# Kernel optimization log

Hardware: AMD Instinct MI355X
Metric: run time of the kernel (lower is better)

Reference implementation:

```python
import jax, jax.numpy as jnp
import numpy as np

B, N, D = 16, 32768, 256
E, H, K, T = 512, 8, 512, 16  # text_embed_dim, nhead, top_k, num_defect_tokens
LN_EPS = 1e-5


def setup_inputs() -> dict:
    key = jax.random.key(0)
    ks = jax.random.split(key, 8)
    sc = 0.02
    return {
        "per_point_features": jax.random.normal(ks[0], (B, N, D), jnp.float32),
        "outlier_scores": jax.random.normal(ks[1], (B, N, 1), jnp.float32),
        "proj_w": jax.random.normal(ks[2], (E, D), jnp.float32) * sc,
        "proj_b": jnp.zeros((E,), jnp.float32),
        "in_proj_w": jax.random.normal(ks[3], (3 * E, E), jnp.float32) * sc,
        "in_proj_b": jnp.zeros((3 * E,), jnp.float32),
        "out_proj_w": jax.random.normal(ks[4], (E, E), jnp.float32) * sc,
        "out_proj_b": jnp.zeros((E,), jnp.float32),
        "ln_g": jnp.ones((E,), jnp.float32),
        "ln_b": jnp.zeros((E,), jnp.float32),
        "ffn_w": jax.random.normal(ks[5], (E, E), jnp.float32) * sc,
        "ffn_b": jnp.zeros((E,), jnp.float32),
    }


def _layernorm(x, g, b):
    mu = jnp.mean(x, axis=-1, keepdims=True)
    var = jnp.mean(jnp.square(x - mu), axis=-1, keepdims=True)
    return (x - mu) * jax.lax.rsqrt(var + LN_EPS) * g + b


def reference(per_point_features, outlier_scores, proj_w, proj_b,
              in_proj_w, in_proj_b, out_proj_w, out_proj_b,
              ln_g, ln_b, ffn_w, ffn_b):
    # top-k select + gather
    scores = outlier_scores[..., 0]                       # [B, N]
    _, idx = jax.lax.top_k(scores, K)                     # [B, K]
    feats = jnp.take_along_axis(per_point_features, idx[:, :, None], axis=1)  # [B, K, D]
    # linear projection to text embed dim
    x = feats @ proj_w.T + proj_b                         # [B, K, E]
    # multi-head self-attention (torch nn.MultiheadAttention semantics)
    qkv = x @ in_proj_w.T + in_proj_b                     # [B, K, 3E]
    q, k, v = jnp.split(qkv, 3, axis=-1)
    dh = E // H
    q = q.reshape(B, K, H, dh)
    k = k.reshape(B, K, H, dh)
    v = v.reshape(B, K, H, dh)
    logits = jnp.einsum("bqhd,bkhd->bhqk", q, k) / np.sqrt(dh).astype(np.float32)
    attn = jax.nn.softmax(logits, axis=-1)
    o = jnp.einsum("bhqk,bkhd->bqhd", attn, v).reshape(B, K, E)
    o = o @ out_proj_w.T + out_proj_b
    # residual + layernorm
    y = _layernorm(x + o, ln_g, ln_b)
    # FFN (linear + exact GELU) with residual
    y = y + jax.nn.gelu(y @ ffn_w.T + ffn_b, approximate=False)
    return y[:, :T, :]                                    # [B, T, E]
```

## Files before the change

kernel.cpp:

```cpp
#include <hip/hip_runtime.h>
#include <hip/hip_bf16.h>
#include <math.h>

#define PB 16
#define PN 32768
#define PD 256
#define PE 512
#define PH 8
#define PK 512
#define PT 16
#define DH 64

typedef __attribute__((ext_vector_type(8))) short bf16x8;
typedef __attribute__((ext_vector_type(4))) float f32x4;

__device__ __forceinline__ unsigned short f2bf(float f) {
    __hip_bfloat16 h = __float2bfloat16(f);
    return *(unsigned short*)&h;
}
__device__ __forceinline__ float b2f(unsigned short u) {
    return __uint_as_float(((unsigned int)u) << 16);
}

__global__ __launch_bounds__(512) void topk_kernel(const float* __restrict__ scores,
                                                   int* __restrict__ sorted_idx) {
    const int b = blockIdx.x;
    const int tid = threadIdx.x;
    const int NT = 512;
    const float* s = scores + (size_t)b * PN;

    __shared__ unsigned int hist[256];
    __shared__ unsigned int sh_prefix;
    __shared__ int sh_remaining;
    __shared__ unsigned int sh_cnt_gt, sh_cnt_eq;
    __shared__ unsigned long long comp[PK];
    __shared__ unsigned int eq_idx[PK];

    unsigned int prefix = 0;
    int remaining = PK;
    for (int shift = 24; shift >= 0; shift -= 8) {
        for (int i = tid; i < 256; i += NT) hist[i] = 0;
        __syncthreads();
        for (int i = tid * 4; i < PN; i += NT * 4) {
            float4 f = *(const float4*)(s + i);
            const float* fp = (const float*)&f;
#pragma unroll
            for (int j = 0; j < 4; ++j) {
                unsigned int u = __float_as_uint(fp[j]);
                u = (u & 0x80000000u) ? ~u : (u | 0x80000000u);
                bool ok = (shift == 24) || ((u >> (shift + 8)) == prefix);
                if (ok) atomicAdd(&hist[(u >> shift) & 0xFFu], 1u);
            }
        }
        __syncthreads();
        if (tid == 0) {
            int cum = 0;
            int d = 255;
            for (; d >= 0; --d) {
                cum += (int)hist[d];
                if (cum >= remaining) break;
            }
            sh_remaining = remaining - (cum - (int)hist[d]);
            sh_prefix = (prefix << 8) | (unsigned)d;
        }
        __syncthreads();
        prefix = sh_prefix;
        remaining = sh_remaining;
        __syncthreads();
    }
    const unsigned int TKEY = prefix;

    if (tid == 0) { sh_cnt_gt = 0; sh_cnt_eq = 0; }
    __syncthreads();
    for (int i = tid * 4; i < PN; i += NT * 4) {
        float4 f = *(const float4*)(s + i);
        const float* fp = (const float*)&f;
#pragma unroll
        for (int j = 0; j < 4; ++j) {
            unsigned int u = __float_as_uint(fp[j]);
            u = (u & 0x80000000u) ? ~u : (u | 0x80000000u);
            if (u > TKEY) {
                unsigned p = atomicAdd(&sh_cnt_gt, 1u);
                comp[p] = ((unsigned long long)u << 32) | (unsigned int)(~(unsigned)(i + j));
            } else if (u == TKEY) {
                unsigned p = atomicAdd(&sh_cnt_eq, 1u);
                if (p < PK) eq_idx[p] = (unsigned)(i + j);
            }
        }
    }
    __syncthreads();
    const int cnt_gt = (int)sh_cnt_gt;
    const int need_eq = PK - cnt_gt;
    const int ec = (int)sh_cnt_eq < PK ? (int)sh_cnt_eq : PK;
    if (tid == 0) {
        for (int j = 0; j < need_eq; ++j) {
            unsigned mv = 0xFFFFFFFFu; int mb = 0;
            for (int i2 = 0; i2 < ec; ++i2)
                if (eq_idx[i2] < mv) { mv = eq_idx[i2]; mb = i2; }
            comp[cnt_gt + j] = ((unsigned long long)TKEY << 32) | (unsigned int)(~mv);
            eq_idx[mb] = 0xFFFFFFFFu;
        }
    }
    __syncthreads();

    for (unsigned ksz = 2; ksz <= PK; ksz <<= 1) {
        for (unsigned j = ksz >> 1; j > 0; j >>= 1) {
            unsigned i = (unsigned)tid;
            unsigned ixj = i ^ j;
            if (ixj > i && i < PK) {
                unsigned long long a = comp[i], c = comp[ixj];
                bool sw = ((i & ksz) == 0) ? (a < c) : (a > c);
                if (sw) { comp[i] = c; comp[ixj] = a; }
            }
            __syncthreads();
        }
    }
    if (tid < PK)
        sorted_idx[b * PK + tid] = (int)(~(unsigned int)(comp[tid] & 0xFFFFFFFFull));
}

__global__ __launch_bounds__(256) void gather_cast_kernel(const float* __restrict__ feats,
                                                          const int* __restrict__ sidx,
                                                          __hip_bfloat16* __restrict__ Ag) {
    const int row = blockIdx.x * 4 + (threadIdx.x >> 6);
    const int lane = threadIdx.x & 63;
    const int b = row >> 9;
    const int src = sidx[row];
    float4 f = *(const float4*)(feats + ((size_t)b * PN + (size_t)src) * PD + lane * 4);
    ushort4 u;
    u.x = f2bf(f.x); u.y = f2bf(f.y); u.z = f2bf(f.z); u.w = f2bf(f.w);
    *(ushort4*)((unsigned short*)Ag + (size_t)row * PD + lane * 4) = u;
}

__global__ __launch_bounds__(256) void cast_weights_kernel(
    const float* __restrict__ proj_w, const float* __restrict__ kv_w,
    __hip_bfloat16* __restrict__ Wp16, __hip_bfloat16* __restrict__ Wkv16) {
    const int n1 = PE * PD / 4;
    const int n2 = 2 * PE * PE / 4;
    int i = blockIdx.x * 256 + threadIdx.x;
    const float4* src;
    unsigned short* dst;
    int off;
    if (i < n1) { src = (const float4*)proj_w; dst = (unsigned short*)Wp16; off = i; }
    else if (i < n1 + n2) { src = (const float4*)kv_w; dst = (unsigned short*)Wkv16; off = i - n1; }
    else return;
    float4 f = src[off];
    ushort4 u;
    u.x = f2bf(f.x); u.y = f2bf(f.y); u.z = f2bf(f.z); u.w = f2bf(f.w);
    *(ushort4*)(dst + (size_t)off * 4) = u;
}

__global__ __launch_bounds__(256) void gemm_bt_bf16_kernel(
    const short* __restrict__ A, const short* __restrict__ Bm,
    const float* __restrict__ bias,
    __hip_bfloat16* __restrict__ C16, float* __restrict__ Xq,
    int M, int N, int Kd) {
    const int tid = threadIdx.x;
    const int wave = tid >> 6;
    const int lane = tid & 63;
    const int m0 = blockIdx.x * 128 + (wave >> 1) * 64;
    const int n0 = blockIdx.y * 128 + (wave & 1) * 64;
    const int mrow = lane & 15;
    const int quad = lane >> 4;

    f32x4 acc[4][4] = {};
    for (int k0 = 0; k0 < Kd; k0 += 32) {
        const int kk = k0 + quad * 8;
        bf16x8 a[4], bf[4];
#pragma unroll
        for (int i = 0; i < 4; ++i)
            a[i] = *(const bf16x8*)(A + (size_t)(m0 + i * 16 + mrow) * Kd + kk);
#pragma unroll
        for (int i = 0; i < 4; ++i)
            bf[i] = *(const bf16x8*)(Bm + (size_t)(n0 + i * 16 + mrow) * Kd + kk);
#pragma unroll
        for (int i = 0; i < 4; ++i)
#pragma unroll
            for (int j = 0; j < 4; ++j)
                acc[i][j] = __builtin_amdgcn_mfma_f32_16x16x32_bf16(a[i], bf[j], acc[i][j], 0, 0, 0);
    }
#pragma unroll
    for (int i = 0; i < 4; ++i)
#pragma unroll
        for (int j = 0; j < 4; ++j)
#pragma unroll
            for (int r = 0; r < 4; ++r) {
                int row = m0 + i * 16 + quad * 4 + r;
                int col = n0 + j * 16 + mrow;
                float v = acc[i][j][r] + bias[col];
                if (C16) {
                    __hip_bfloat16 hv = __float2bfloat16(v);
                    ((__hip_bfloat16*)C16)[(size_t)row * N + col] = hv;
                }
                if (Xq) {
                    int t = row & (PK - 1);
                    if (t < PT)
                        Xq[((size_t)(row >> 9) * PT + t) * N + col] = v;
                }
            }
}

__global__ __launch_bounds__(256) void sgemm_bt_kernel(
    const float* __restrict__ A, const float* __restrict__ Bm,
    const float* __restrict__ bias, const float* __restrict__ resid,
    float* __restrict__ C, int M, int N, int Kd) {
    __shared__ float As[32][33];
    __shared__ float Bs[32][33];
    const int tid = threadIdx.x;
    const int m0 = blockIdx.x * 32, n0 = blockIdx.y * 32;
    const int tx = tid & 15, ty = tid >> 4;
    float acc00 = 0, acc01 = 0, acc10 = 0, acc11 = 0;
    for (int k0 = 0; k0 < Kd; k0 += 32) {
        for (int e = tid; e < 1024; e += 256) {
            int r = e >> 5, c = e & 31;
            As[r][c] = A[(size_t)(m0 + r) * Kd + k0 + c];
            Bs[r][c] = Bm[(size_t)(n0 + r) * Kd + k0 + c];
        }
        __syncthreads();
#pragma unroll
        for (int kk = 0; kk < 32; ++kk) {
            float a0 = As[ty * 2][kk], a1 = As[ty * 2 + 1][kk];
            float b0 = Bs[tx * 2][kk], b1 = Bs[tx * 2 + 1][kk];
            acc00 += a0 * b0; acc01 += a0 * b1;
            acc10 += a1 * b0; acc11 += a1 * b1;
        }
        __syncthreads();
    }
    float bc0 = bias[n0 + tx * 2], bc1 = bias[n0 + tx * 2 + 1];
    float v00 = acc00 + bc0, v01 = acc01 + bc1, v10 = acc10 + bc0, v11 = acc11 + bc1;
    size_t i00 = (size_t)(m0 + ty * 2) * N + n0 + tx * 2;
    size_t i10 = (size_t)(m0 + ty * 2 + 1) * N + n0 + tx * 2;
    if (resid) {
        v00 = resid[i00]     + 0.5f * v00 * (1.0f + erff(v00 * 0.7071067811865475f));
        v01 = resid[i00 + 1] + 0.5f * v01 * (1.0f + erff(v01 * 0.7071067811865475f));
        v10 = resid[i10]     + 0.5f * v10 * (1.0f + erff(v10 * 0.7071067811865475f));
        v11 = resid[i10 + 1] + 0.5f * v11 * (1.0f + erff(v11 * 0.7071067811865475f));
    }
    C[i00] = v00; C[i00 + 1] = v01;
    C[i10] = v10; C[i10 + 1] = v11;
}

__global__ __launch_bounds__(256) void attn_kernel(
    const float* __restrict__ qb, const __hip_bfloat16* __restrict__ kv,
    float* __restrict__ ob) {
    const int bh = blockIdx.x;
    const int b = bh >> 3, h = bh & 7;
    const int tid = threadIdx.x;
    __shared__ float qs[PT][DH + 4];
    __shared__ float ls[PT][PK + 1];

    {
        int i4 = tid * 4;
        int t = i4 >> 6, d = i4 & 63;
        float4 f = *(const float4*)(qb + (size_t)(b * PT + t) * PE + h * DH + d);
        qs[t][d] = f.x; qs[t][d + 1] = f.y; qs[t][d + 2] = f.z; qs[t][d + 3] = f.w;
    }
    __syncthreads();

    const int t = tid >> 4;
    const int ko = tid & 15;
    for (int k = ko; k < PK; k += 16) {
        const ushort4* kp = (const ushort4*)((const unsigned short*)kv +
                             (size_t)(b * PK + k) * (2 * PE) + h * DH);
        float acc = 0;
#pragma unroll
        for (int c = 0; c < 16; ++c) {
            ushort4 vv = kp[c];
            acc += qs[t][c * 4 + 0] * b2f(vv.x) + qs[t][c * 4 + 1] * b2f(vv.y)
                 + qs[t][c * 4 + 2] * b2f(vv.z) + qs[t][c * 4 + 3] * b2f(vv.w);
        }
        ls[t][k] = acc * 0.125f;
    }
    float m = -1e30f;
    for (int k = ko; k < PK; k += 16) m = fmaxf(m, ls[t][k]);
#pragma unroll
    for (int s = 8; s >= 1; s >>= 1) m = fmaxf(m, __shfl_xor(m, s, 16));
    float sum = 0;
    for (int k = ko; k < PK; k += 16) {
        float e = __expf(ls[t][k] - m);
        ls[t][k] = e;
        sum += e;
    }
#pragma unroll
    for (int s = 8; s >= 1; s >>= 1) sum += __shfl_xor(sum, s, 16);
    const float inv = 1.0f / sum;

    const int d0 = (tid & 15) * 4;
    const unsigned short* vbase = (const unsigned short*)kv +
                                  (size_t)(b * PK) * (2 * PE) + PE + h * DH + d0;
    float o0 = 0, o1 = 0, o2 = 0, o3 = 0;
#pragma unroll 4
    for (int k = 0; k < PK; ++k) {
        float w = ls[t][k];
        ushort4 vv = *(const ushort4*)(vbase + (size_t)k * (2 * PE));
        o0 += w * b2f(vv.x); o1 += w * b2f(vv.y);
        o2 += w * b2f(vv.z); o3 += w * b2f(vv.w);
    }
    float4 o; o.x = o0 * inv; o.y = o1 * inv; o.z = o2 * inv; o.w = o3 * inv;
    *(float4*)(ob + (size_t)(b * PT + t) * PE + h * DH + d0) = o;
}

__global__ __launch_bounds__(256) void ln_kernel(
    const float* __restrict__ xq, const float* __restrict__ o2,
    const float* __restrict__ g, const float* __restrict__ bb,
    float* __restrict__ y) {
    const int r = blockIdx.x;
    const int tid = threadIdx.x;
    __shared__ float red[4], red2[4];
    float v0 = xq[(size_t)r * PE + tid] + o2[(size_t)r * PE + tid];
    float v1 = xq[(size_t)r * PE + 256 + tid] + o2[(size_t)r * PE + 256 + tid];
    float s = v0 + v1;
#pragma unroll
    for (int sh = 32; sh >= 1; sh >>= 1) s += __shfl_xor(s, sh, 64);
    if ((tid & 63) == 0) red[tid >> 6] = s;
    __syncthreads();
    float mean = (red[0] + red[1] + red[2] + red[3]) * (1.0f / 512.0f);
    float d0 = v0 - mean, d1 = v1 - mean;
    float sq = d0 * d0 + d1 * d1;
#pragma unroll
    for (int sh = 32; sh >= 1; sh >>= 1) sq += __shfl_xor(sq, sh, 64);
    if ((tid & 63) == 0) red2[tid >> 6] = sq;
    __syncthreads();
    float var = (red2[0] + red2[1] + red2[2] + red2[3]) * (1.0f / 512.0f);
    float rs = rsqrtf(var + 1e-5f);
    y[(size_t)r * PE + tid]       = d0 * rs * g[tid] + bb[tid];
    y[(size_t)r * PE + 256 + tid] = d1 * rs * g[tid + 256] + bb[tid + 256];
}

extern "C" void kernel_launch(void* const* d_in, const int* in_sizes, int n_in,
                              void* d_out, int out_size, void* d_ws, size_t ws_size,
                              hipStream_t stream) {
    const float* feats  = (const float*)d_in[0];
    const float* scores = (const float*)d_in[1];
    const float* proj_w = (const float*)d_in[2];
    const float* proj_b = (const float*)d_in[3];
    const float* in_w   = (const float*)d_in[4];
    const float* in_b   = (const float*)d_in[5];
    const float* out_w  = (const float*)d_in[6];
    const float* out_b  = (const float*)d_in[7];
    const float* ln_g   = (const float*)d_in[8];
    const float* ln_b   = (const float*)d_in[9];
    const float* ffn_w  = (const float*)d_in[10];
    const float* ffn_b  = (const float*)d_in[11];
    float* out = (float*)d_out;

    char* p = (char*)d_ws;
    auto alloc = [&](size_t bytes) {
        void* r = (void*)p;
        p += (bytes + 255) & ~(size_t)255;
        return r;
    };
    int* sidx             = (int*)alloc((size_t)PB * PK * 4);
    __hip_bfloat16* Ag    = (__hip_bfloat16*)alloc((size_t)PB * PK * PD * 2);
    __hip_bfloat16* Wp16  = (__hip_bfloat16*)alloc((size_t)PE * PD * 2);
    __hip_bfloat16* Wkv16 = (__hip_bfloat16*)alloc((size_t)2 * PE * PE * 2);
    __hip_bfloat16* x16   = (__hip_bfloat16*)alloc((size_t)PB * PK * PE * 2);
    __hip_bfloat16* kv16  = (__hip_bfloat16*)alloc((size_t)PB * PK * 2 * PE * 2);
    float* xq             = (float*)alloc((size_t)PB * PT * PE * 4);
    float* qb             = (float*)alloc((size_t)PB * PT * PE * 4);
    float* ob             = (float*)alloc((size_t)PB * PT * PE * 4);
    float* o2             = (float*)alloc((size_t)PB * PT * PE * 4);
    float* yb             = (float*)alloc((size_t)PB * PT * PE * 4);
    if ((size_t)(p - (char*)d_ws) > ws_size) return;

    topk_kernel<<<PB, 512, 0, stream>>>(scores, sidx);
    gather_cast_kernel<<<PB * PK / 4, 256, 0, stream>>>(feats, sidx, Ag);
    {
        int nvec = (PE * PD + 2 * PE * PE) / 4;
        cast_weights_kernel<<<(nvec + 255) / 256, 256, 0, stream>>>(
            proj_w, in_w + (size_t)PE * PE, Wp16, Wkv16);
    }
    gemm_bt_bf16_kernel<<<dim3(64, 4), 256, 0, stream>>>(
        (const short*)Ag, (const short*)Wp16, proj_b, x16, xq, PB * PK, PE, PD);
    gemm_bt_bf16_kernel<<<dim3(64, 8), 256, 0, stream>>>(
        (const short*)x16, (const short*)Wkv16, in_b + PE, kv16, nullptr,
        PB * PK, 2 * PE, PE);
    sgemm_bt_kernel<<<dim3(8, 16), 256, 0, stream>>>(xq, in_w, in_b, nullptr, qb, PB * PT, PE, PE);
    attn_kernel<<<PB * PH, 256, 0, stream>>>(qb, kv16, ob);
    sgemm_bt_kernel<<<dim3(8, 16), 256, 0, stream>>>(ob, out_w, out_b, nullptr, o2, PB * PT, PE, PE);
    ln_kernel<<<PB * PT, 256, 0, stream>>>(xq, o2, ln_g, ln_b, yb);
    sgemm_bt_kernel<<<dim3(8, 16), 256, 0, stream>>>(yb, ffn_w, ffn_b, yb, out, PB * PT, PE, PE);
}
```

Measured before the change: 909.0 us.

## Fold input projection into KV weights and fuse gather/cast/weight prep

Precomputes the combined weight W_kv·proj_w (1024x256) and combined bias in a single prep kernel that also does the gather/cast. This removes the full 8192x512 projection GEMM and the x16 intermediate, so the KV GEMM runs over K=256 directly from the gathered features. The x rows for the first T tokens are now computed by a small fp32 GEMM, and the Q projection moves into the attention kernel. The top-k histogram threshold search becomes a parallel suffix scan instead of a serial loop on one thread. The composed weight is rounded to bf16 after the fold, which changes numerics slightly.

```diff
diff --git a/kernel.cpp b/kernel.cpp
--- a/kernel.cpp
+++ b/kernel.cpp
@@ -30,6 +30,7 @@
     const float* s = scores + (size_t)b * PN;
 
     __shared__ unsigned int hist[256];
+    __shared__ unsigned int scan_buf[256];
     __shared__ unsigned int sh_prefix;
     __shared__ int sh_remaining;
     __shared__ unsigned int sh_cnt_gt, sh_cnt_eq;
@@ -53,15 +54,22 @@
             }
         }
         __syncthreads();
-        if (tid == 0) {
-            int cum = 0;
-            int d = 255;
-            for (; d >= 0; --d) {
-                cum += (int)hist[d];
-                if (cum >= remaining) break;
-            }
-            sh_remaining = remaining - (cum - (int)hist[d]);
-            sh_prefix = (prefix << 8) | (unsigned)d;
+        if (tid < 256) scan_buf[tid] = hist[tid];
+        __syncthreads();
+        for (int off = 1; off < 256; off <<= 1) {
+            unsigned int add = 0;
+            if (tid < 256 - off) add = scan_buf[tid + off];
+            __syncthreads();
+            if (tid < 256) scan_buf[tid] += add;
+            __syncthreads();
+        }
+        if (tid < 256) {
+            int suf = (int)scan_buf[tid];
+            int sufn = (tid < 255) ? (int)scan_buf[tid + 1] : 0;
+            if (suf >= remaining && sufn < remaining) {
+                sh_prefix = (prefix << 8) | (unsigned)tid;
+                sh_remaining = remaining - sufn;
+            }
         }
         __syncthreads();
         prefix = sh_prefix;
@@ -119,41 +127,77 @@
         sorted_idx[b * PK + tid] = (int)(~(unsigned int)(comp[tid] & 0xFFFFFFFFull));
 }
 
-__global__ __launch_bounds__(256) void gather_cast_kernel(const float* __restrict__ feats,
-                                                          const int* __restrict__ sidx,
-                                                          __hip_bfloat16* __restrict__ Ag) {
-    const int row = blockIdx.x * 4 + (threadIdx.x >> 6);
-    const int lane = threadIdx.x & 63;
-    const int b = row >> 9;
-    const int src = sidx[row];
-    float4 f = *(const float4*)(feats + ((size_t)b * PN + (size_t)src) * PD + lane * 4);
-    ushort4 u;
-    u.x = f2bf(f.x); u.y = f2bf(f.y); u.z = f2bf(f.z); u.w = f2bf(f.w);
-    *(ushort4*)((unsigned short*)Ag + (size_t)row * PD + lane * 4) = u;
-}
-
-__global__ __launch_bounds__(256) void cast_weights_kernel(
-    const float* __restrict__ proj_w, const float* __restrict__ kv_w,
-    __hip_bfloat16* __restrict__ Wp16, __hip_bfloat16* __restrict__ Wkv16) {
-    const int n1 = PE * PD / 4;
-    const int n2 = 2 * PE * PE / 4;
-    int i = blockIdx.x * 256 + threadIdx.x;
-    const float4* src;
-    unsigned short* dst;
-    int off;
-    if (i < n1) { src = (const float4*)proj_w; dst = (unsigned short*)Wp16; off = i; }
-    else if (i < n1 + n2) { src = (const float4*)kv_w; dst = (unsigned short*)Wkv16; off = i - n1; }
-    else return;
-    float4 f = src[off];
-    ushort4 u;
-    u.x = f2bf(f.x); u.y = f2bf(f.y); u.z = f2bf(f.z); u.w = f2bf(f.w);
-    *(ushort4*)(dst + (size_t)off * 4) = u;
+__global__ __launch_bounds__(256) void prep_kernel(
+    const float* __restrict__ feats, const int* __restrict__ sidx,
+    const float* __restrict__ proj_w, const float* __restrict__ proj_b,
+    const float* __restrict__ in_w, const float* __restrict__ in_b,
+    __hip_bfloat16* __restrict__ Ag, float* __restrict__ Aq,
+    __hip_bfloat16* __restrict__ Wc16, float* __restrict__ b_comb) {
+    const int blk = blockIdx.x;
+    const int tid = threadIdx.x;
+    __shared__ float As[32][33];
+    __shared__ float Bs[32][33];
+
+    if (blk < 2048) {
+        const int row = blk * 4 + (tid >> 6);
+        const int lane = tid & 63;
+        const int b = row >> 9, t = row & (PK - 1);
+        const int src = sidx[row];
+        float4 f = *(const float4*)(feats + ((size_t)b * PN + (size_t)src) * PD + lane * 4);
+        ushort4 u;
+        u.x = f2bf(f.x); u.y = f2bf(f.y); u.z = f2bf(f.z); u.w = f2bf(f.w);
+        *(ushort4*)((unsigned short*)Ag + (size_t)row * PD + lane * 4) = u;
+        if (t < PT)
+            *(float4*)(Aq + (size_t)(b * PT + t) * PD + lane * 4) = f;
+    } else if (blk < 2048 + 256) {
+        const int bb = blk - 2048;
+        const int m0 = (bb >> 3) * 32, n0 = (bb & 7) * 32;
+        const float* A = in_w + (size_t)PE * PE;
+        const int tx = tid & 15, ty = tid >> 4;
+        float a00 = 0, a01 = 0, a10 = 0, a11 = 0;
+        for (int k0 = 0; k0 < PE; k0 += 32) {
+            for (int e = tid; e < 1024; e += 256) {
+                int r = e >> 5, c = e & 31;
+                As[r][c] = A[(size_t)(m0 + r) * PE + k0 + c];
+                Bs[r][c] = proj_w[(size_t)(k0 + r) * PD + n0 + c];
+            }
+            __syncthreads();
+#pragma unroll
+            for (int kk = 0; kk < 32; ++kk) {
+                float x0 = As[ty * 2][kk], x1 = As[ty * 2 + 1][kk];
+                float y0 = Bs[kk][tx * 2], y1 = Bs[kk][tx * 2 + 1];
+                a00 += x0 * y0; a01 += x0 * y1;
+                a10 += x1 * y0; a11 += x1 * y1;
+            }
+            __syncthreads();
+        }
+        __hip_bfloat16* W = Wc16;
+        W[(size_t)(m0 + ty * 2) * PD + n0 + tx * 2]         = __float2bfloat16(a00);
+        W[(size_t)(m0 + ty * 2) * PD + n0 + tx * 2 + 1]     = __float2bfloat16(a01);
+        W[(size_t)(m0 + ty * 2 + 1) * PD + n0 + tx * 2]     = __float2bfloat16(a10);
+        W[(size_t)(m0 + ty * 2 + 1) * PD + n0 + tx * 2 + 1] = __float2bfloat16(a11);
+    } else {
+        const int bi = blk - 2304;
+        const int rr = tid >> 4, ko = tid & 15;
+        const int row = bi * 16 + rr;
+        const float* wrow = in_w + (size_t)PE * PE + (size_t)row * PE;
+        float acc = 0;
+#pragma unroll
+        for (int c = 0; c < 8; ++c) {
+            int e = c * 64 + ko * 4;
+            float4 w4 = *(const float4*)(wrow + e);
+            float4 b4 = *(const float4*)(proj_b + e);
+            acc += w4.x * b4.x + w4.y * b4.y + w4.z * b4.z + w4.w * b4.w;
+        }
+#pragma unroll
+        for (int sft = 8; sft >= 1; sft >>= 1) acc += __shfl_xor(acc, sft, 16);
+        if (ko == 0) b_comb[row] = acc + in_b[PE + row];
+    }
 }
 
 __global__ __launch_bounds__(256) void gemm_bt_bf16_kernel(
     const short* __restrict__ A, const short* __restrict__ Bm,
-    const float* __restrict__ bias,
-    __hip_bfloat16* __restrict__ C16, float* __restrict__ Xq,
+    const float* __restrict__ bias, __hip_bfloat16* __restrict__ C16,
     int M, int N, int Kd) {
     const int tid = threadIdx.x;
     const int wave = tid >> 6;
@@ -187,16 +231,7 @@
             for (int r = 0; r < 4; ++r) {
                 int row = m0 + i * 16 + quad * 4 + r;
                 int col = n0 + j * 16 + mrow;
-                float v = acc[i][j][r] + bias[col];
-                if (C16) {
-                    __hip_bfloat16 hv = __float2bfloat16(v);
-                    ((__hip_bfloat16*)C16)[(size_t)row * N + col] = hv;
-                }
-                if (Xq) {
-                    int t = row & (PK - 1);
-                    if (t < PT)
-                        Xq[((size_t)(row >> 9) * PT + t) * N + col] = v;
-                }
+                C16[(size_t)row * N + col] = __float2bfloat16(acc[i][j][r] + bias[col]);
             }
 }
 
@@ -241,19 +276,44 @@
 }
 
 __global__ __launch_bounds__(256) void attn_kernel(
-    const float* __restrict__ qb, const __hip_bfloat16* __restrict__ kv,
+    const float* __restrict__ xq, const float* __restrict__ in_w,
+    const float* __restrict__ in_b, const __hip_bfloat16* __restrict__ kv,
     float* __restrict__ ob) {
     const int bh = blockIdx.x;
     const int b = bh >> 3, h = bh & 7;
     const int tid = threadIdx.x;
+    __shared__ float xs[PT][PE + 4];
     __shared__ float qs[PT][DH + 4];
     __shared__ float ls[PT][PK + 1];
 
+#pragma unroll
+    for (int i = 0; i < 8; ++i) {
+        int idx = tid * 4 + i * 1024;
+        int t = idx >> 9, e = idx & 511;
+        float4 f = *(const float4*)(xq + (size_t)(b * PT + t) * PE + e);
+        *(float4*)&xs[t][e] = f;
+    }
+    __syncthreads();
+
     {
-        int i4 = tid * 4;
-        int t = i4 >> 6, d = i4 & 63;
-        float4 f = *(const float4*)(qb + (size_t)(b * PT + t) * PE + h * DH + d);
-        qs[t][d] = f.x; qs[t][d + 1] = f.y; qs[t][d + 2] = f.z; qs[t][d + 3] = f.w;
+        const int t = tid >> 4, d0 = (tid & 15) * 4;
+        const float* w0 = in_w + (size_t)(h * DH + d0) * PE;
+        float a0 = 0, a1 = 0, a2 = 0, a3 = 0;
+        for (int e = 0; e < PE; e += 4) {
+            float4 xv = *(const float4*)&xs[t][e];
+            float4 w4a = *(const float4*)(w0 + e);
+            float4 w4b = *(const float4*)(w0 + PE + e);
+            float4 w4c = *(const float4*)(w0 + 2 * PE + e);
+            float4 w4d = *(const float4*)(w0 + 3 * PE + e);
+            a0 += xv.x * w4a.x + xv.y * w4a.y + xv.z * w4a.z + xv.w * w4a.w;
+            a1 += xv.x * w4b.x + xv.y * w4b.y + xv.z * w4b.z + xv.w * w4b.w;
+            a2 += xv.x * w4c.x + xv.y * w4c.y + xv.z * w4c.z + xv.w * w4c.w;
+            a3 += xv.x * w4d.x + xv.y * w4d.y + xv.z * w4d.z + xv.w * w4d.w;
+        }
+        qs[t][d0]     = a0 + in_b[h * DH + d0];
+        qs[t][d0 + 1] = a1 + in_b[h * DH + d0 + 1];
+        qs[t][d0 + 2] = a2 + in_b[h * DH + d0 + 2];
+        qs[t][d0 + 3] = a3 + in_b[h * DH + d0 + 3];
     }
     __syncthreads();
 
@@ -352,32 +412,27 @@
     };
     int* sidx             = (int*)alloc((size_t)PB * PK * 4);
     __hip_bfloat16* Ag    = (__hip_bfloat16*)alloc((size_t)PB * PK * PD * 2);
-    __hip_bfloat16* Wp16  = (__hip_bfloat16*)alloc((size_t)PE * PD * 2);
-    __hip_bfloat16* Wkv16 = (__hip_bfloat16*)alloc((size_t)2 * PE * PE * 2);
-    __hip_bfloat16* x16   = (__hip_bfloat16*)alloc((size_t)PB * PK * PE * 2);
+    float* Aq             = (float*)alloc((size_t)PB * PT * PD * 4);
+    __hip_bfloat16* Wc16  = (__hip_bfloat16*)alloc((size_t)2 * PE * PD * 2);
+    float* b_comb         = (float*)alloc((size_t)2 * PE * 4);
     __hip_bfloat16* kv16  = (__hip_bfloat16*)alloc((size_t)PB * PK * 2 * PE * 2);
     float* xq             = (float*)alloc((size_t)PB * PT * PE * 4);
-    float* qb             = (float*)alloc((size_t)PB * PT * PE * 4);
     float* ob             = (float*)alloc((size_t)PB * PT * PE * 4);
     float* o2             = (float*)alloc((size_t)PB * PT * PE * 4);
     float* yb             = (float*)alloc((size_t)PB * PT * PE * 4);
     if ((size_t)(p - (char*)d_ws) > ws_size) return;
 
     topk_kernel<<<PB, 512, 0, stream>>>(scores, sidx);
-    gather_cast_kernel<<<PB * PK / 4, 256, 0, stream>>>(feats, sidx, Ag);
-    {
-        int nvec = (PE * PD + 2 * PE * PE) / 4;
-        cast_weights_kernel<<<(nvec + 255) / 256, 256, 0, stream>>>(
-            proj_w, in_w + (size_t)PE * PE, Wp16, Wkv16);
-    }
-    gemm_bt_bf16_kernel<<<dim3(64, 4), 256, 0, stream>>>(
-        (const short*)Ag, (const short*)Wp16, proj_b, x16, xq, PB * PK, PE, PD);
+    prep_kernel<<<2048 + 256 + 64, 256, 0, stream>>>(
+        feats, sidx, proj_w, proj_b, in_w, in_b, Ag, Aq, Wc16, b_comb);
     gemm_bt_bf16_kernel<<<dim3(64, 8), 256, 0, stream>>>(
-        (const short*)x16, (const short*)Wkv16, in_b + PE, kv16, nullptr,
-        PB * PK, 2 * PE, PE);
-    sgemm_bt_kernel<<<dim3(8, 16), 256, 0, stream>>>(xq, in_w, in_b, nullptr, qb, PB * PT, PE, PE);
-    attn_kernel<<<PB * PH, 256, 0, stream>>>(qb, kv16, ob);
-    sgemm_bt_kernel<<<dim3(8, 16), 256, 0, stream>>>(ob, out_w, out_b, nullptr, o2, PB * PT, PE, PE);
+        (const short*)Ag, (const short*)Wc16, b_comb, kv16, PB * PK, 2 * PE, PD);
+    sgemm_bt_kernel<<<dim3(8, 16), 256, 0, stream>>>(Aq, proj_w, proj_b, nullptr, xq,
+                                                     PB * PT, PE, PD);
+    attn_kernel<<<PB * PH, 256, 0, stream>>>(xq, in_w, in_b, kv16, ob);
+    sgemm_bt_kernel<<<dim3(8, 16), 256, 0, stream>>>(ob, out_w, out_b, nullptr, o2,
+                                                     PB * PT, PE, PE);
     ln_kernel<<<PB * PT, 256, 0, stream>>>(xq, o2, ln_g, ln_b, yb);
-    sgemm_bt_kernel<<<dim3(8, 16), 256, 0, stream>>>(yb, ffn_w, ffn_b, yb, out, PB * PT, PE, PE);
-}
+    sgemm_bt_kernel<<<dim3(8, 16), 256, 0, stream>>>(yb, ffn_w, ffn_b, yb, out,
+                                                     PB * PT, PE, PE);
+}
```

New measurement: 960.8 us. 5.7% more time.
